# Performance work log

Hardware: AMD Instinct MI355X
Metric: run time of the kernel (lower is better)

The kernel has to match this reference:

```python
import jax, jax.numpy as jnp
import numpy as np

HIDDEN = 16


def setup_inputs() -> dict:
    key = jax.random.key(0)
    ks = jax.random.split(key, 7)
    B, T = 16384, 2048
    s_ih = 1.0 / np.sqrt(HIDDEN)
    x = jax.random.normal(ks[0], (B, T, 1), dtype=jnp.float32)
    # PyTorch GRU param layout: weight_ih [3H, in], weight_hh [3H, H], biases [3H]
    w_ih = jax.random.uniform(ks[1], (3 * HIDDEN, 1), jnp.float32, -s_ih, s_ih)
    w_hh = jax.random.uniform(ks[2], (3 * HIDDEN, HIDDEN), jnp.float32, -s_ih, s_ih)
    b_ih = jax.random.uniform(ks[3], (3 * HIDDEN,), jnp.float32, -s_ih, s_ih)
    b_hh = jax.random.uniform(ks[4], (3 * HIDDEN,), jnp.float32, -s_ih, s_ih)
    w_fc = jax.random.uniform(ks[5], (1, HIDDEN), jnp.float32, -s_ih, s_ih)
    b_fc = jax.random.uniform(ks[6], (1,), jnp.float32, -s_ih, s_ih)
    return {"x": x, "w_ih": w_ih, "w_hh": w_hh, "b_ih": b_ih, "b_hh": b_hh,
            "w_fc": w_fc, "b_fc": b_fc}


def reference(x, w_ih, w_hh, b_ih, b_hh, w_fc, b_fc):
    H = HIDDEN
    B = x.shape[0]
    # Precompute input projections for all timesteps: [B, T, 3H]
    gi_all = jnp.einsum('bti,gi->btg', x, w_ih) + b_ih
    gi_all = jnp.transpose(gi_all, (1, 0, 2))  # [T, B, 3H] for scan

    def step(h, gi):
        gh = h @ w_hh.T + b_hh  # [B, 3H]
        r = jax.nn.sigmoid(gi[:, :H] + gh[:, :H])
        z = jax.nn.sigmoid(gi[:, H:2 * H] + gh[:, H:2 * H])
        n = jnp.tanh(gi[:, 2 * H:] + r * gh[:, 2 * H:])
        h_new = (1.0 - z) * n + z * h
        return h_new, None

    h0 = jnp.zeros((B, H), dtype=x.dtype)
    h_last, _ = jax.lax.scan(step, h0, gi_all)
    # fc on last timestep output (== final hidden state)
    return h_last @ w_fc.T + b_fc  # [B, 1]
```

## Files before the change

### kernel.cpp

```cpp
#include <hip/hip_runtime.h>
#include <hip/hip_bf16.h>

#define HID 16
#define TLEN 2048
#define WIN 64
#define NW (TLEN / WIN)
#define RSTR 68

typedef float f32x4 __attribute__((ext_vector_type(4)));
typedef short s16x8 __attribute__((ext_vector_type(8)));
typedef unsigned int u32x4 __attribute__((ext_vector_type(4)));

#if __has_builtin(__builtin_amdgcn_exp2f)
#define EXP2(x) __builtin_amdgcn_exp2f(x)
#else
#define EXP2(x) __builtin_exp2f(x)
#endif
#if __has_builtin(__builtin_amdgcn_rcpf)
#define RCP(x) __builtin_amdgcn_rcpf(x)
#else
#define RCP(x) (1.0f / (x))
#endif

__device__ __forceinline__ unsigned int pack_bf16(float a, float b) {
    float2 t; t.x = a; t.y = b;
    __hip_bfloat162 p = __float22bfloat162_rn(t);
    unsigned int r;
    __builtin_memcpy(&r, &p, 4);
    return r;
}

__device__ __forceinline__ float sigm2(float u) {
    return RCP(1.0f + EXP2(u));
}

__global__ __launch_bounds__(256) void gru_fused(
    const float* __restrict__ x, const float* __restrict__ w_ih,
    const float* __restrict__ w_hh, const float* __restrict__ b_ih,
    const float* __restrict__ b_hh, const float* __restrict__ w_fc,
    const float* __restrict__ b_fc, float* __restrict__ out)
{
    __shared__ float xs[4][2][16 * RSTR];

    const int tid  = threadIdx.x;
    const int wv   = tid >> 6;
    const int lane = tid & 63;
    const int sidx = lane & 15;
    const int grp  = lane >> 4;
    const int seq0 = (blockIdx.x * 4 + wv) * 16;

    const float LOG2E = 1.4426950408889634f;
    const float sc[3] = {LOG2E, LOG2E, 2.0f * LOG2E};

    s16x8 afr[3];
    f32x4 cini[3];
    float wih0[4], wih1[4], wih2[4], bin[4];
    #pragma unroll
    for (int q = 0; q < 3; ++q) {
        const float s = -sc[q];
        const float* wrow = w_hh + (q * 16 + sidx) * HID + grp * 4;
        u32x4 ua;
        ua.x = pack_bf16(s * wrow[0], s * wrow[1]);
        ua.y = pack_bf16(s * wrow[2], s * wrow[3]);
        ua.z = 0u; ua.w = 0u;
        afr[q] = __builtin_bit_cast(s16x8, ua);
        #pragma unroll
        for (int r = 0; r < 4; ++r) {
            int g = q * 16 + grp * 4 + r;
            float bias = b_hh[g] + (q < 2 ? b_ih[g] : 0.0f);
            cini[q][r] = s * bias;
            float w = s * w_ih[g];
            if (q == 0) wih0[r] = w; else if (q == 1) wih1[r] = w; else wih2[r] = w;
        }
    }
    #pragma unroll
    for (int r = 0; r < 4; ++r) bin[r] = -sc[2] * b_ih[32 + grp * 4 + r];

    const float* xbase = x + (size_t)(seq0 + sidx) * TLEN + grp * 16;
    const int woff = sidx * RSTR + grp * 16;
    const int roff = sidx * RSTR;

    float* cur = &xs[wv][0][0];
    float* nxt = &xs[wv][1][0];

    f32x4 pf0 = *(const f32x4*)(xbase + 0);
    f32x4 pf1 = *(const f32x4*)(xbase + 4);
    f32x4 pf2 = *(const f32x4*)(xbase + 8);
    f32x4 pf3 = *(const f32x4*)(xbase + 12);
    *(f32x4*)(cur + woff + 0)  = pf0;
    *(f32x4*)(cur + woff + 4)  = pf1;
    *(f32x4*)(cur + woff + 8)  = pf2;
    *(f32x4*)(cur + woff + 12) = pf3;

    float h[4] = {0.f, 0.f, 0.f, 0.f};
    s16x8 bfr;
    { u32x4 z; z.x = 0u; z.y = 0u; z.z = 0u; z.w = 0u;
      bfr = __builtin_bit_cast(s16x8, z); }

    float xcur = cur[roff];

    for (int w = 0; w < NW; ++w) {
        const bool more = (w + 1 < NW);
        if (more) {
            const float* xb = xbase + (w + 1) * WIN;
            pf0 = *(const f32x4*)(xb + 0);
            pf1 = *(const f32x4*)(xb + 4);
            pf2 = *(const f32x4*)(xb + 8);
            pf3 = *(const f32x4*)(xb + 12);
        }
        #pragma unroll 4
        for (int tt = 0; tt < WIN; ++tt) {
            float xnext = cur[roff + ((tt + 1) & (WIN - 1))];

            f32x4 c0 = __builtin_amdgcn_mfma_f32_16x16x32_bf16(afr[0], bfr, cini[0], 0, 0, 0);
            f32x4 c1 = __builtin_amdgcn_mfma_f32_16x16x32_bf16(afr[1], bfr, cini[1], 0, 0, 0);
            f32x4 c2 = __builtin_amdgcn_mfma_f32_16x16x32_bf16(afr[2], bfr, cini[2], 0, 0, 0);

            #pragma unroll
            for (int i = 0; i < 4; ++i) {
                float rr = sigm2(fmaf(xcur, wih0[i], c0[i]));
                float zz = sigm2(fmaf(xcur, wih1[i], c1[i]));
                float un = fmaf(xcur, wih2[i], bin[i]);
                un = fmaf(rr, c2[i], un);
                float nn = fmaf(2.0f, sigm2(un), -1.0f);
                h[i] = fmaf(zz, h[i] - nn, nn);
            }
            u32x4 uu;
            uu.x = pack_bf16(h[0], h[1]);
            uu.y = pack_bf16(h[2], h[3]);
            uu.z = 0u; uu.w = 0u;
            bfr = __builtin_bit_cast(s16x8, uu);
            xcur = xnext;
        }
        if (more) {
            *(f32x4*)(nxt + woff + 0)  = pf0;
            *(f32x4*)(nxt + woff + 4)  = pf1;
            *(f32x4*)(nxt + woff + 8)  = pf2;
            *(f32x4*)(nxt + woff + 12) = pf3;
            float* t = cur; cur = nxt; nxt = t;
            xcur = cur[roff];
        }
    }

    float p = h[0] * w_fc[grp * 4 + 0] + h[1] * w_fc[grp * 4 + 1] +
              h[2] * w_fc[grp * 4 + 2] + h[3] * w_fc[grp * 4 + 3];
    p += __shfl_xor(p, 16, 64);
    p += __shfl_xor(p, 32, 64);
    if (grp == 0) out[seq0 + sidx] = p + b_fc[0];
}

extern "C" void kernel_launch(void* const* d_in, const int* in_sizes, int n_in,
                              void* d_out, int out_size, void* d_ws, size_t ws_size,
                              hipStream_t stream) {
    const float* x    = (const float*)d_in[0];
    const float* w_ih = (const float*)d_in[1];
    const float* w_hh = (const float*)d_in[2];
    const float* b_ih = (const float*)d_in[3];
    const float* b_hh = (const float*)d_in[4];
    const float* w_fc = (const float*)d_in[5];
    const float* b_fc = (const float*)d_in[6];
    float* out = (float*)d_out;

    const int B = in_sizes[0] / TLEN;
    dim3 grid(B / 64), block(256);
    gru_fused<<<grid, block, 0, stream>>>(x, w_ih, w_hh, b_ih, b_hh, w_fc, b_fc, out);
}
```

Before: 561.5 us.

## Replace sigmoid/tanh transcendental calls with LDS piecewise-linear lookup tables

Builds 256-entry piecewise-linear tables for sigmoid and tanh in shared memory at kernel start. The per-step exp2/rcp transcendentals are replaced by a clamp, an index computation, an LDS load and an FMA. The pre-scaling of weights by -log2e is dropped, and the inner unroll goes from 4 to 2. This approximates the activations with limited accuracy (step 1/16, clamped to [-8,8]) and puts dependent LDS load latency on the serial recurrence path.

Result: slower. 731.1 us (+30.2%).

```diff
diff --git a/kernel.cpp b/kernel.cpp
--- a/kernel.cpp
+++ b/kernel.cpp
@@ -1,5 +1,6 @@
 #include <hip/hip_runtime.h>
 #include <hip/hip_bf16.h>
+#include <math.h>
 
 #define HID 16
 #define TLEN 2048
@@ -7,19 +8,20 @@
 #define NW (TLEN / WIN)
 #define RSTR 68
 
+#define TSEG 256
+#define TLO  (-8.0f)
+#define THI  (7.9375f)
+#define TSCL 16.0f
+#define TBIAS 128.0f
+
 typedef float f32x4 __attribute__((ext_vector_type(4)));
 typedef short s16x8 __attribute__((ext_vector_type(8)));
 typedef unsigned int u32x4 __attribute__((ext_vector_type(4)));
 
-#if __has_builtin(__builtin_amdgcn_exp2f)
-#define EXP2(x) __builtin_amdgcn_exp2f(x)
+#if __has_builtin(__builtin_amdgcn_fmed3f)
+#define CLAMP3(x, lo, hi) __builtin_amdgcn_fmed3f((x), (lo), (hi))
 #else
-#define EXP2(x) __builtin_exp2f(x)
-#endif
-#if __has_builtin(__builtin_amdgcn_rcpf)
-#define RCP(x) __builtin_amdgcn_rcpf(x)
-#else
-#define RCP(x) (1.0f / (x))
+#define CLAMP3(x, lo, hi) fminf(fmaxf((x), (lo)), (hi))
 #endif
 
 __device__ __forceinline__ unsigned int pack_bf16(float a, float b) {
@@ -30,10 +32,6 @@
     return r;
 }
 
-__device__ __forceinline__ float sigm2(float u) {
-    return RCP(1.0f + EXP2(u));
-}
-
 __global__ __launch_bounds__(256) void gru_fused(
     const float* __restrict__ x, const float* __restrict__ w_ih,
     const float* __restrict__ w_hh, const float* __restrict__ b_ih,
@@ -41,40 +39,51 @@
     const float* __restrict__ b_fc, float* __restrict__ out)
 {
     __shared__ float xs[4][2][16 * RSTR];
+    __shared__ float2 sig_tab[TSEG];
+    __shared__ float2 tanh_tab[TSEG];
 
     const int tid  = threadIdx.x;
+
+    {
+        const float x0 = TLO + (float)tid * (1.0f / TSCL);
+        const float x1 = x0 + (1.0f / TSCL);
+        float s0 = 1.0f / (1.0f + __expf(-x0));
+        float s1 = 1.0f / (1.0f + __expf(-x1));
+        float sl = (s1 - s0) * TSCL;
+        sig_tab[tid] = make_float2(fmaf(-sl, x0, s0), sl);
+        float t0 = tanhf(x0), t1 = tanhf(x1);
+        float tl = (t1 - t0) * TSCL;
+        tanh_tab[tid] = make_float2(fmaf(-tl, x0, t0), tl);
+    }
+    __syncthreads();
+
     const int wv   = tid >> 6;
     const int lane = tid & 63;
     const int sidx = lane & 15;
     const int grp  = lane >> 4;
     const int seq0 = (blockIdx.x * 4 + wv) * 16;
 
-    const float LOG2E = 1.4426950408889634f;
-    const float sc[3] = {LOG2E, LOG2E, 2.0f * LOG2E};
-
     s16x8 afr[3];
     f32x4 cini[3];
     float wih0[4], wih1[4], wih2[4], bin[4];
     #pragma unroll
     for (int q = 0; q < 3; ++q) {
-        const float s = -sc[q];
         const float* wrow = w_hh + (q * 16 + sidx) * HID + grp * 4;
         u32x4 ua;
-        ua.x = pack_bf16(s * wrow[0], s * wrow[1]);
-        ua.y = pack_bf16(s * wrow[2], s * wrow[3]);
+        ua.x = pack_bf16(wrow[0], wrow[1]);
+        ua.y = pack_bf16(wrow[2], wrow[3]);
         ua.z = 0u; ua.w = 0u;
         afr[q] = __builtin_bit_cast(s16x8, ua);
         #pragma unroll
         for (int r = 0; r < 4; ++r) {
             int g = q * 16 + grp * 4 + r;
-            float bias = b_hh[g] + (q < 2 ? b_ih[g] : 0.0f);
-            cini[q][r] = s * bias;
-            float w = s * w_ih[g];
+            cini[q][r] = b_hh[g] + (q < 2 ? b_ih[g] : 0.0f);
+            float w = w_ih[g];
             if (q == 0) wih0[r] = w; else if (q == 1) wih1[r] = w; else wih2[r] = w;
         }
     }
     #pragma unroll
-    for (int r = 0; r < 4; ++r) bin[r] = -sc[2] * b_ih[32 + grp * 4 + r];
+    for (int r = 0; r < 4; ++r) bin[r] = b_ih[32 + grp * 4 + r];
 
     const float* xbase = x + (size_t)(seq0 + sidx) * TLEN + grp * 16;
     const int woff = sidx * RSTR + grp * 16;
@@ -108,7 +117,7 @@
             pf2 = *(const f32x4*)(xb + 8);
             pf3 = *(const f32x4*)(xb + 12);
         }
-        #pragma unroll 4
+        #pragma unroll 2
         for (int tt = 0; tt < WIN; ++tt) {
             float xnext = cur[roff + ((tt + 1) & (WIN - 1))];
 
@@ -116,13 +125,34 @@
             f32x4 c1 = __builtin_amdgcn_mfma_f32_16x16x32_bf16(afr[1], bfr, cini[1], 0, 0, 0);
             f32x4 c2 = __builtin_amdgcn_mfma_f32_16x16x32_bf16(afr[2], bfr, cini[2], 0, 0, 0);
 
+            float uc_r[4], uc_z[4];
+            float2 er[4], ez[4];
             #pragma unroll
             for (int i = 0; i < 4; ++i) {
-                float rr = sigm2(fmaf(xcur, wih0[i], c0[i]));
-                float zz = sigm2(fmaf(xcur, wih1[i], c1[i]));
+                float ur = fmaf(xcur, wih0[i], c0[i]);
+                uc_r[i] = CLAMP3(ur, TLO, THI);
+                er[i] = sig_tab[(int)fmaf(uc_r[i], TSCL, TBIAS)];
+            }
+            #pragma unroll
+            for (int i = 0; i < 4; ++i) {
+                float uz = fmaf(xcur, wih1[i], c1[i]);
+                uc_z[i] = CLAMP3(uz, TLO, THI);
+                ez[i] = sig_tab[(int)fmaf(uc_z[i], TSCL, TBIAS)];
+            }
+            float uc_n[4];
+            float2 en[4];
+            #pragma unroll
+            for (int i = 0; i < 4; ++i) {
+                float rr = fmaf(er[i].y, uc_r[i], er[i].x);
                 float un = fmaf(xcur, wih2[i], bin[i]);
                 un = fmaf(rr, c2[i], un);
-                float nn = fmaf(2.0f, sigm2(un), -1.0f);
+                uc_n[i] = CLAMP3(un, TLO, THI);
+                en[i] = tanh_tab[(int)fmaf(uc_n[i], TSCL, TBIAS)];
+            }
+            #pragma unroll
+            for (int i = 0; i < 4; ++i) {
+                float zz = fmaf(ez[i].y, uc_z[i], ez[i].x);
+                float nn = fmaf(en[i].y, uc_n[i], en[i].x);
                 h[i] = fmaf(zz, h[i] - nn, nn);
             }
             u32x4 uu;
```
